# Kernel optimization log

Hardware: AMD Instinct MI355X
Metric: run time of the kernel (lower is better)

Reference implementation:

```python
import jax, jax.numpy as jnp
import numpy as np

N, D = 8192, 512
NUM_SOURCES = 8


def setup_inputs() -> dict:
    key = jax.random.key(0)
    k1, k2, k3 = jax.random.split(key, 3)
    image_features = jax.random.normal(k1, (N, D), dtype=jnp.float32)
    text_features = jax.random.normal(k2, (N, D), dtype=jnp.float32)
    logit_scale = jnp.ones((), dtype=jnp.float32)
    source_labels = jax.random.randint(k3, (N,), 0, NUM_SOURCES, dtype=jnp.int64)
    return {
        "image_features": image_features,
        "text_features": text_features,
        "logit_scale": logit_scale,
        "source_labels": source_labels,
    }


def reference(image_features, text_features, logit_scale, source_labels):
    n = source_labels.shape[0]
    # [N, N] logits and row-wise log-softmax
    logits = logit_scale * (image_features @ text_features.T)
    log_probs = jax.nn.log_softmax(logits, axis=1)
    # same-source mask, diagonal excluded
    mask = (source_labels[:, None] == source_labels[None, :]) & (~jnp.eye(n, dtype=bool))
    count_pos = mask.sum(axis=1)  # [N]
    row_sum = jnp.where(mask, log_probs, 0.0).sum(axis=1)  # [N]
    # per-row mean over positives; rows with zero positives contribute 0
    row_mean = jnp.where(count_pos > 0, row_sum / jnp.maximum(count_pos, 1).astype(log_probs.dtype), 0.0)
    # loss = -(sum_i row_mean_i) / N
    return -row_mean.sum() / n
```

## Files before the change

kernel.cpp:

```cpp
#include <hip/hip_runtime.h>
#include <cmath>

#define NN 8192
#define DD 512
#define NSRC 8
#define PSW 8
#define COFF 100.0f

typedef __bf16 bf16x8 __attribute__((ext_vector_type(8)));
typedef float  f32x4  __attribute__((ext_vector_type(4)));

__device__ __forceinline__ unsigned short f2bf(float f) {
    unsigned u = __float_as_uint(f);
    u += 0x7fffu + ((u >> 16) & 1u);
    return (unsigned short)(u >> 16);
}

__global__ __launch_bounds__(256) void k_prep(
    const float* __restrict__ img, const float* __restrict__ txt,
    const int* __restrict__ labels,
    unsigned short* __restrict__ imgB, unsigned short* __restrict__ txtB,
    float* __restrict__ Tsum, int* __restrict__ counts)
{
    const int tid = threadIdx.x;
    if (blockIdx.x >= 128) {
        const size_t gid = (size_t)(blockIdx.x - 128) * 256 + tid;
        const size_t half = (size_t)NN * DD / 8;
        const float* src = (gid < half) ? img : txt;
        unsigned short* dst = (gid < half) ? imgB : txtB;
        const size_t off = ((gid < half) ? gid : gid - half) * 8;
        const float4 v0 = *(const float4*)(src + off);
        const float4 v1 = *(const float4*)(src + off + 4);
        union { unsigned short s[8]; uint4 v; } o;
        o.s[0] = f2bf(v0.x); o.s[1] = f2bf(v0.y); o.s[2] = f2bf(v0.z); o.s[3] = f2bf(v0.w);
        o.s[4] = f2bf(v1.x); o.s[5] = f2bf(v1.y); o.s[6] = f2bf(v1.z); o.s[7] = f2bf(v1.w);
        *(uint4*)(dst + off) = o.v;
        return;
    }
    __shared__ float Tacc[NSRC * DD];
    __shared__ int cacc[NSRC];
    const int d0 = 2 * tid;
#pragma unroll
    for (int s = 0; s < NSRC; s++) {
        Tacc[s * DD + d0] = 0.f;
        Tacc[s * DD + d0 + 1] = 0.f;
    }
    if (tid < NSRC) cacc[tid] = 0;
    __syncthreads();

    const int row0 = blockIdx.x * 64;
    if (tid < 64) atomicAdd(&cacc[labels[row0 + tid]], 1);

    for (int j = 0; j < 64; j++) {
        const int lab = labels[row0 + j];
        const float2 v = *(const float2*)(txt + (size_t)(row0 + j) * DD + d0);
        Tacc[lab * DD + d0]     += v.x;
        Tacc[lab * DD + d0 + 1] += v.y;
    }
    __syncthreads();
#pragma unroll
    for (int k = 0; k < NSRC * DD / 256; k++) {
        const int e = k * 256 + tid;
        atomicAdd(&Tsum[e], Tacc[e]);
    }
    if (tid < NSRC) atomicAdd(&counts[tid], cacc[tid]);
}

__global__ __launch_bounds__(512, 2) void k_lse_mfma256(
    const unsigned short* __restrict__ imgB, const unsigned short* __restrict__ txtB,
    const float* __restrict__ scale_p, float* __restrict__ ps)
{
    __shared__ uint4 lds[8192];
    const float scale = scale_p[0];
    const int tid  = threadIdx.x;
    const int lane = tid & 63;
    const int w    = tid >> 6;
    const int wr   = w >> 2;
    const int wc   = w & 3;
    const int lq   = lane >> 4;
    const int ln   = lane & 15;
    const int c    = blockIdx.x & 7;
    const int l    = blockIdx.x >> 3;
    const int by   = c * 4 + (l >> 3);
    const int bcg  = l & 7;
    const int row0    = by * 256;
    const int colBase = bcg * 1024;

    const int st_r  = tid >> 3;
    const int st_kc = (tid & 7) ^ (st_r & 7);
    const int xsw   = ln & 7;

    int rowA[2][4], colB[2][2];
#pragma unroll
    for (int ih = 0; ih < 2; ih++)
#pragma unroll
        for (int ii = 0; ii < 4; ii++)
            rowA[ih][ii] = (wr * 128 + ih * 64 + ii * 16 + ln) * 8;
#pragma unroll
    for (int jh = 0; jh < 2; jh++)
#pragma unroll
        for (int jj = 0; jj < 2; jj++)
            colB[jh][jj] = (wc * 64 + jh * 32 + jj * 16 + ln) * 8;

#define SA(BUF, Q, T)                                                          \
    { const unsigned short* g = imgB + (size_t)(row0 + (Q) * 64 + st_r) * DD   \
          + (((T) & 7) << 6) + (st_kc << 3);                                   \
      __builtin_amdgcn_global_load_lds(                                        \
          (const __attribute__((address_space(1))) void*)g,                    \
          (__attribute__((address_space(3))) void*)                            \
              &lds[(BUF) * 4096 + (Q) * 512 + tid], 16, 0, 0); }
#define SB(BUF, Q, T)                                                          \
    { const unsigned short* g = txtB                                           \
          + (size_t)(colBase + ((((T) >> 3) & 3) << 8) + (Q) * 64 + st_r) * DD \
          + (((T) & 7) << 6) + (st_kc << 3);                                   \
      __builtin_amdgcn_global_load_lds(                                        \
          (const __attribute__((address_space(1))) void*)g,                    \
          (__attribute__((address_space(3))) void*)                            \
              &lds[(BUF) * 4096 + 2048 + (Q) * 512 + tid], 16, 0, 0); }

#define PHASE_(BUF, IH, JH, RA, STG, VM)                                       \
    do {                                                                       \
        if (RA) {                                                              \
            _Pragma("unroll") for (int ii = 0; ii < 4; ii++) {                 \
                _Pragma("unroll") for (int ks = 0; ks < 2; ks++) {             \
                    af[ii][ks] = *reinterpret_cast<const bf16x8*>(             \
                        &lds[(BUF) * 4096 + rowA[IH][ii]                       \
                             + (((ks << 2) + lq) ^ xsw)]);                     \
                }                                                              \
            }                                                                  \
        }                                                                      \
        bf16x8 bf[2][2];                                                       \
        _Pragma("unroll") for (int jj = 0; jj < 2; jj++) {                     \
            _Pragma("unroll") for (int ks = 0; ks < 2; ks++) {                 \
                bf[jj][ks] = *reinterpret_cast<const bf16x8*>(                 \
                    &lds[(BUF) * 4096 + 2048 + colB[JH][jj]                    \
                         + (((ks << 2) + lq) ^ xsw)]);                         \
            }                                                                  \
        }                                                                      \
        STG;                                                                   \
        __builtin_amdgcn_s_barrier();                                          \
        asm volatile("s_waitcnt lgkmcnt(0)" ::: "memory");                     \
        __builtin_amdgcn_sched_barrier(0);                                     \
        __builtin_amdgcn_s_setprio(1);                                         \
        _Pragma("unroll") for (int ks = 0; ks < 2; ks++) {                     \
            _Pragma("unroll") for (int ii = 0; ii < 4; ii++) {                 \
                _Pragma("unroll") for (int jj = 0; jj < 2; jj++) {             \
                    acc[(IH) * 4 + ii][(JH) * 2 + jj] =                        \
                        __builtin_amdgcn_mfma_f32_16x16x32_bf16(               \
                            af[ii][ks], bf[jj][ks],                            \
                            acc[(IH) * 4 + ii][(JH) * 2 + jj], 0, 0, 0);       \
                }                                                              \
            }                                                                  \
        }                                                                      \
        __builtin_amdgcn_s_setprio(0);                                         \
        if (VM) { asm volatile("s_waitcnt vmcnt(2)" ::: "memory"); }           \
        __builtin_amdgcn_s_barrier();                                          \
    } while (0)

#pragma unroll
    for (int q = 0; q < 4; q++) SA(0, q, 0);
#pragma unroll
    for (int q = 0; q < 4; q++) SB(0, q, 0);
    SA(1, 0, 1); SA(1, 2, 1);
    asm volatile("s_waitcnt vmcnt(2)" ::: "memory");
    __builtin_amdgcn_s_barrier();

    f32x4 acc[8][4];
    f32x4 s_run[8];
#pragma unroll
    for (int i = 0; i < 8; i++) {
        s_run[i] = (f32x4){0.f, 0.f, 0.f, 0.f};
#pragma unroll
        for (int j = 0; j < 4; j++) acc[i][j] = (f32x4){0.f, 0.f, 0.f, 0.f};
    }
    bf16x8 af[4][2];

#pragma unroll 1
    for (int v0 = 0; v0 < 32; v0 += 2) {
        PHASE_(0, 0, 0, 1, SA(1, 1, v0 + 1); SA(1, 3, v0 + 1), 0);
        PHASE_(0, 0, 1, 0, SB(1, 0, v0 + 1); SB(1, 1, v0 + 1), 0);
        PHASE_(0, 1, 0, 1, SB(1, 2, v0 + 1); SB(1, 3, v0 + 1), 0);
        PHASE_(0, 1, 1, 0, SA(0, 0, v0 + 2); SA(0, 2, v0 + 2), 1);
        PHASE_(1, 0, 0, 1, SA(0, 1, v0 + 2); SA(0, 3, v0 + 2), 0);
        PHASE_(1, 0, 1, 0, SB(0, 0, v0 + 2); SB(0, 1, v0 + 2), 0);
        PHASE_(1, 1, 0, 1, SB(0, 2, v0 + 2); SB(0, 3, v0 + 2), 0);
        PHASE_(1, 1, 1, 0, SA(1, 0, v0 + 3); SA(1, 2, v0 + 3), 1);
        if ((v0 & 6) == 6) {
#pragma unroll
            for (int i = 0; i < 8; i++) {
#pragma unroll
                for (int rg = 0; rg < 4; rg++) {
                    float es = s_run[i][rg];
#pragma unroll
                    for (int j = 0; j < 4; j++)
                        es += __expf(fmaf(acc[i][j][rg], scale, -COFF));
                    s_run[i][rg] = es;
                }
#pragma unroll
                for (int j = 0; j < 4; j++)
                    acc[i][j] = (f32x4){0.f, 0.f, 0.f, 0.f};
            }
        }
    }

    asm volatile("s_waitcnt vmcnt(0)" ::: "memory");
    __syncthreads();

    float* fred = (float*)lds;
#pragma unroll
    for (int i = 0; i < 8; i++) {
#pragma unroll
        for (int rg = 0; rg < 4; rg++) {
            float es = s_run[i][rg];
#pragma unroll
            for (int off = 8; off; off >>= 1) es += __shfl_xor(es, off);
            if (ln == 0)
                fred[(wr * 128 + i * 16 + lq * 4 + rg) * 4 + wc] = es;
        }
    }
    __syncthreads();
    if (tid < 256) {
        const float tot = fred[tid * 4] + fred[tid * 4 + 1]
                        + fred[tid * 4 + 2] + fred[tid * 4 + 3];
        ps[(size_t)(row0 + tid) * PSW + bcg] = tot;
    }
#undef SA
#undef SB
#undef PHASE_
}

__global__ __launch_bounds__(256) void k_finalize(
    const float* __restrict__ img, const float* __restrict__ txt,
    const int* __restrict__ labels, const float* __restrict__ scale_p,
    const float* __restrict__ Tsum, const int* __restrict__ counts,
    const float* __restrict__ ps,
    float* __restrict__ out)
{
    const float scale = scale_p[0];
    const int tid = threadIdx.x;
    const int lane = tid & 63;
    const int wave = tid >> 6;
    const int rowBase = blockIdx.x * 16 + wave * 4;
    float local = 0.f;
#pragma unroll
    for (int it = 0; it < 4; it++) {
        const int i = rowBase + it;
        const int lab = labels[i];
        float ds = 0.f, dt = 0.f;
        const float* ip = img + (size_t)i * DD;
        const float* tp = txt + (size_t)i * DD;
        const float* sp = Tsum + lab * DD;
#pragma unroll
        for (int k = lane; k < DD; k += 64) {
            const float a = ip[k];
            ds = fmaf(a, tp[k], ds);
            dt = fmaf(a, sp[k], dt);
        }
        float es = (lane < PSW) ? ps[(size_t)i * PSW + lane] : 0.f;
#pragma unroll
        for (int off = 32; off; off >>= 1) {
            ds += __shfl_xor(ds, off);
            dt += __shfl_xor(dt, off);
            es += __shfl_xor(es, off);
        }
        if (lane == 0) {
            const float lse = COFF + __logf(es);
            const int cnt = counts[lab] - 1;
            if (cnt > 0) {
                const float row_sum = scale * (dt - ds) - (float)cnt * lse;
                local += row_sum / (float)cnt;
            }
        }
    }
    __shared__ float red[4];
    if (lane == 0) red[wave] = local;
    __syncthreads();
    if (tid == 0) {
        const float t = red[0] + red[1] + red[2] + red[3];
        atomicAdd(out, -t / (float)NN);
    }
}

extern "C" void kernel_launch(void* const* d_in, const int* in_sizes, int n_in,
                              void* d_out, int out_size, void* d_ws, size_t ws_size,
                              hipStream_t stream)
{
    const float* img     = (const float*)d_in[0];
    const float* txt     = (const float*)d_in[1];
    const float* scale_p = (const float*)d_in[2];
    const int*   labels  = (const int*)d_in[3];
    float* out = (float*)d_out;

    char* ws = (char*)d_ws;
    float* ps    = (float*)(ws);
    float* Tsum  = (float*)(ws + (1 << 18));
    int*   counts = (int*)(ws + (1 << 18) + NSRC * DD * 4);
    unsigned short* imgB = (unsigned short*)(ws + 2 * 1024 * 1024);
    unsigned short* txtB = (unsigned short*)(ws + 10 * 1024 * 1024);

    hipMemsetAsync(ws + (1 << 18), 0, NSRC * DD * 4 + 64, stream);
    hipMemsetAsync(d_out, 0, 4, stream);

    k_prep<<<128 + (2 * NN * DD / 8) / 256, 256, 0, stream>>>(
        img, txt, labels, imgB, txtB, Tsum, counts);
    k_lse_mfma256<<<256, 512, 0, stream>>>(imgB, txtB, scale_p, ps);
    k_finalize<<<NN / 16, 256, 0, stream>>>(img, txt, labels, scale_p,
                                            Tsum, counts, ps, out);
}
```

Before: 177.6 us.

## Fuse prep, LSE GEMM, and finalize into one persistent kernel with grid barriers

Merges the three kernels (bf16 conversion plus per-source text sums, the MFMA log-sum-exp pass, and the finalize reduction) into one 256-block kernel. A global atomic spin barrier separates the prep phase from the GEMM. Per-panel counters let each row panel finalize once its eight column blocks are done, and a last-block-done pattern writes the scalar output. This removes two kernel launches, one memset, and the tail gaps between kernels. In exchange it relies on all 256 blocks being co-resident (at 2 blocks per CU) and adds spin-wait overhead, with a risk of deadlock if residency does not hold.

```diff
diff --git a/kernel.cpp b/kernel.cpp
--- a/kernel.cpp
+++ b/kernel.cpp
@@ -16,62 +16,16 @@
     return (unsigned short)(u >> 16);
 }
 
-__global__ __launch_bounds__(256) void k_prep(
+__global__ __launch_bounds__(512, 2) void k_fused(
     const float* __restrict__ img, const float* __restrict__ txt,
-    const int* __restrict__ labels,
+    const int* __restrict__ labels, const float* __restrict__ scale_p,
     unsigned short* __restrict__ imgB, unsigned short* __restrict__ txtB,
-    float* __restrict__ Tsum, int* __restrict__ counts)
-{
-    const int tid = threadIdx.x;
-    if (blockIdx.x >= 128) {
-        const size_t gid = (size_t)(blockIdx.x - 128) * 256 + tid;
-        const size_t half = (size_t)NN * DD / 8;
-        const float* src = (gid < half) ? img : txt;
-        unsigned short* dst = (gid < half) ? imgB : txtB;
-        const size_t off = ((gid < half) ? gid : gid - half) * 8;
-        const float4 v0 = *(const float4*)(src + off);
-        const float4 v1 = *(const float4*)(src + off + 4);
-        union { unsigned short s[8]; uint4 v; } o;
-        o.s[0] = f2bf(v0.x); o.s[1] = f2bf(v0.y); o.s[2] = f2bf(v0.z); o.s[3] = f2bf(v0.w);
-        o.s[4] = f2bf(v1.x); o.s[5] = f2bf(v1.y); o.s[6] = f2bf(v1.z); o.s[7] = f2bf(v1.w);
-        *(uint4*)(dst + off) = o.v;
-        return;
-    }
-    __shared__ float Tacc[NSRC * DD];
-    __shared__ int cacc[NSRC];
-    const int d0 = 2 * tid;
-#pragma unroll
-    for (int s = 0; s < NSRC; s++) {
-        Tacc[s * DD + d0] = 0.f;
-        Tacc[s * DD + d0 + 1] = 0.f;
-    }
-    if (tid < NSRC) cacc[tid] = 0;
-    __syncthreads();
-
-    const int row0 = blockIdx.x * 64;
-    if (tid < 64) atomicAdd(&cacc[labels[row0 + tid]], 1);
-
-    for (int j = 0; j < 64; j++) {
-        const int lab = labels[row0 + j];
-        const float2 v = *(const float2*)(txt + (size_t)(row0 + j) * DD + d0);
-        Tacc[lab * DD + d0]     += v.x;
-        Tacc[lab * DD + d0 + 1] += v.y;
-    }
-    __syncthreads();
-#pragma unroll
-    for (int k = 0; k < NSRC * DD / 256; k++) {
-        const int e = k * 256 + tid;
-        atomicAdd(&Tsum[e], Tacc[e]);
-    }
-    if (tid < NSRC) atomicAdd(&counts[tid], cacc[tid]);
-}
-
-__global__ __launch_bounds__(512, 2) void k_lse_mfma256(
-    const unsigned short* __restrict__ imgB, const unsigned short* __restrict__ txtB,
-    const float* __restrict__ scale_p, float* __restrict__ ps)
+    unsigned* __restrict__ sync_cnt, unsigned* __restrict__ panel_cnt,
+    unsigned* __restrict__ done_cnt, float* __restrict__ ws_acc,
+    float* __restrict__ Tsum, int* __restrict__ counts,
+    float* __restrict__ ps, float* __restrict__ out)
 {
     __shared__ uint4 lds[8192];
-    const float scale = scale_p[0];
     const int tid  = threadIdx.x;
     const int lane = tid & 63;
     const int w    = tid >> 6;
@@ -86,6 +40,51 @@
     const int row0    = by * 256;
     const int colBase = bcg * 1024;
 
+    {
+        const size_t half = (size_t)NN * DD / 8;
+#pragma unroll
+        for (int cch = 0; cch < 8; cch++) {
+            const size_t gid = (size_t)blockIdx.x * 4096 + (size_t)cch * 512 + tid;
+            const float* src = (gid < half) ? img : txt;
+            unsigned short* dst = (gid < half) ? imgB : txtB;
+            const size_t off = ((gid < half) ? gid : gid - half) * 8;
+            const float4 v0 = *(const float4*)(src + off);
+            const float4 v1 = *(const float4*)(src + off + 4);
+            union { unsigned short s[8]; uint4 v; } o;
+            o.s[0] = f2bf(v0.x); o.s[1] = f2bf(v0.y); o.s[2] = f2bf(v0.z); o.s[3] = f2bf(v0.w);
+            o.s[4] = f2bf(v1.x); o.s[5] = f2bf(v1.y); o.s[6] = f2bf(v1.z); o.s[7] = f2bf(v1.w);
+            *(uint4*)(dst + off) = o.v;
+        }
+    }
+    if (blockIdx.x < 128) {
+        const int r0 = blockIdx.x * 64;
+        float accs[NSRC];
+#pragma unroll
+        for (int s = 0; s < NSRC; s++) accs[s] = 0.f;
+#pragma unroll 8
+        for (int j = 0; j < 64; j++) {
+            const int lab = labels[r0 + j];
+            const float v = txt[(size_t)(r0 + j) * DD + tid];
+#pragma unroll
+            for (int s = 0; s < NSRC; s++)
+                accs[s] += (lab == s) ? v : 0.f;
+        }
+#pragma unroll
+        for (int s = 0; s < NSRC; s++)
+            atomicAdd(&Tsum[s * DD + tid], accs[s]);
+        if (tid < 64) atomicAdd(&counts[labels[r0 + tid]], 1);
+    }
+
+    __syncthreads();
+    if (tid == 0) {
+        __threadfence();
+        atomicAdd(sync_cnt, 1u);
+        while (atomicAdd(sync_cnt, 0u) < 256u) __builtin_amdgcn_s_sleep(8);
+        __threadfence();
+    }
+    __syncthreads();
+
+    const float scale = scale_p[0];
     const int st_r  = tid >> 3;
     const int st_kc = (tid & 7) ^ (st_r & 7);
     const int xsw   = ln & 7;
@@ -227,24 +226,21 @@
 #undef SA
 #undef SB
 #undef PHASE_
-}
-
-__global__ __launch_bounds__(256) void k_finalize(
-    const float* __restrict__ img, const float* __restrict__ txt,
-    const int* __restrict__ labels, const float* __restrict__ scale_p,
-    const float* __restrict__ Tsum, const int* __restrict__ counts,
-    const float* __restrict__ ps,
-    float* __restrict__ out)
-{
-    const float scale = scale_p[0];
-    const int tid = threadIdx.x;
-    const int lane = tid & 63;
-    const int wave = tid >> 6;
-    const int rowBase = blockIdx.x * 16 + wave * 4;
+
+    __syncthreads();
+    if (tid == 0) {
+        __threadfence();
+        atomicAdd(&panel_cnt[by], 1u);
+        while (atomicAdd(&panel_cnt[by], 0u) < 8u) __builtin_amdgcn_s_sleep(8);
+        __threadfence();
+    }
+    __syncthreads();
+
     float local = 0.f;
+    const int rowF = row0 + bcg * 32 + w * 4;
 #pragma unroll
     for (int it = 0; it < 4; it++) {
-        const int i = rowBase + it;
+        const int i = rowF + it;
         const int lab = labels[i];
         float ds = 0.f, dt = 0.f;
         const float* ip = img + (size_t)i * DD;
@@ -272,12 +268,21 @@
             }
         }
     }
-    __shared__ float red[4];
-    if (lane == 0) red[wave] = local;
+    float* red = (float*)lds + 2048;
+    if (lane == 0) red[w] = local;
     __syncthreads();
     if (tid == 0) {
-        const float t = red[0] + red[1] + red[2] + red[3];
-        atomicAdd(out, -t / (float)NN);
+        float tot = 0.f;
+#pragma unroll
+        for (int i = 0; i < 8; i++) tot += red[i];
+        atomicAdd(ws_acc, tot);
+        __threadfence();
+        const unsigned o = atomicAdd(done_cnt, 1u);
+        if (o == 255u) {
+            __threadfence();
+            const float v = atomicAdd(ws_acc, 0.0f);
+            out[0] = -v / (float)NN;
+        }
     }
 }
 
@@ -292,18 +297,20 @@
     float* out = (float*)d_out;
 
     char* ws = (char*)d_ws;
-    float* ps    = (float*)(ws);
-    float* Tsum  = (float*)(ws + (1 << 18));
-    int*   counts = (int*)(ws + (1 << 18) + NSRC * DD * 4);
+    unsigned* sync_cnt  = (unsigned*)(ws + 0);
+    unsigned* done_cnt  = (unsigned*)(ws + 4);
+    float*    ws_acc    = (float*)(ws + 8);
+    unsigned* panel_cnt = (unsigned*)(ws + 64);
+    float*    Tsum      = (float*)(ws + 256);
+    int*      counts    = (int*)(ws + 256 + NSRC * DD * 4);
+    float*    ps        = (float*)(ws + 32768);
     unsigned short* imgB = (unsigned short*)(ws + 2 * 1024 * 1024);
     unsigned short* txtB = (unsigned short*)(ws + 10 * 1024 * 1024);
 
-    hipMemsetAsync(ws + (1 << 18), 0, NSRC * DD * 4 + 64, stream);
-    hipMemsetAsync(d_out, 0, 4, stream);
-
-    k_prep<<<128 + (2 * NN * DD / 8) / 256, 256, 0, stream>>>(
-        img, txt, labels, imgB, txtB, Tsum, counts);
-    k_lse_mfma256<<<256, 512, 0, stream>>>(imgB, txtB, scale_p, ps);
-    k_finalize<<<NN / 16, 256, 0, stream>>>(img, txt, labels, scale_p,
-                                            Tsum, counts, ps, out);
+    hipMemsetAsync(ws, 0, 256 + NSRC * DD * 4 + 64, stream);
+
+    k_fused<<<256, 512, 0, stream>>>(img, txt, labels, scale_p,
+                                     imgB, txtB,
+                                     sync_cnt, panel_cnt, done_cnt, ws_acc,
+                                     Tsum, counts, ps, out);
 }
```

Measured after the change: 235.7 us. 32.7% more time.
